# Kernel tuning notes

Hardware: AMD Instinct MI355X
Metric: run time of the kernel (lower is better)

## Reference

```python
import jax, jax.numpy as jnp
import numpy as np

B, QL, DL, RSZ, T = 16, 32, 12, 500, 2
DW, DH = 256, 512
HP = DH // 2  # per-direction GRU hidden
NW, NE = 50000, 100000


def _gru_dir(xp, mask, Wh, bh, reverse):
    # xp: [B, L, 3H'] precomputed input projections; mask: [B, L, 1]
    Hp = Wh.shape[1]
    xp_t = jnp.swapaxes(xp, 0, 1)
    m_t = jnp.swapaxes(mask, 0, 1)
    h0 = jnp.zeros((xp.shape[0], Hp), xp.dtype)

    def step(h, inp):
        x, m = inp
        gh = h @ Wh.T + bh
        r = jax.nn.sigmoid(x[:, :Hp] + gh[:, :Hp])
        z = jax.nn.sigmoid(x[:, Hp:2 * Hp] + gh[:, Hp:2 * Hp])
        n = jnp.tanh(x[:, 2 * Hp:] + r * gh[:, 2 * Hp:])
        hn = (1.0 - z) * n + z * h
        h = m * hn + (1.0 - m) * h  # skip updates at pad tokens
        return h, h

    hT, hs = jax.lax.scan(step, h0, (xp_t, m_t), reverse=reverse)
    return jnp.swapaxes(hs, 0, 1), hT


def _bigru(tokens, emb, Wx, Wh, bx, bh):
    # tokens: [B, L] int, 0 = pad. Wx: [2, 3H', D], Wh: [2, 3H', H'], bx/bh: [2, 3H']
    x = emb[tokens]
    mask = (tokens != 0).astype(x.dtype)[..., None]
    xp_f = jnp.einsum('bld,gd->blg', x, Wx[0]) + bx[0]
    xp_b = jnp.einsum('bld,gd->blg', x, Wx[1]) + bx[1]
    hs_f, hT_f = _gru_dir(xp_f, mask, Wh[0], bh[0], False)
    hs_b, hT_b = _gru_dir(xp_b, mask, Wh[1], bh[1], True)
    word_h = jnp.concatenate([hs_f, hs_b], -1) * mask  # zero pad positions
    sent = jnp.concatenate([hT_f, hT_b], -1)  # last fwd / last bwd hidden
    return word_h, sent


def setup_inputs() -> dict:
    key = jax.random.key(0)
    ks = jax.random.split(key, 12)

    def gru_p(k, din):
        k1, k2 = jax.random.split(k, 2)
        s = 1.0 / float(np.sqrt(HP))
        return (jax.random.normal(k1, (2, 3 * HP, din), jnp.float32) * s,
                jax.random.normal(k2, (2, 3 * HP, HP), jnp.float32) * s,
                jnp.zeros((2, 3 * HP), jnp.float32),
                jnp.zeros((2, 3 * HP), jnp.float32))

    q_Wx, q_Wh, q_bx, q_bh = gru_p(ks[0], DW)
    d_Wx, d_Wh, d_bx, d_bh = gru_p(ks[1], DW)
    kaim = float(np.sqrt(2.0 / DH))
    return {
        'questions': jax.random.randint(ks[2], (B, QL), 0, NW),
        'e_s': jax.random.uniform(ks[3], (B, NE), jnp.float32),
        'pair': jax.random.randint(ks[4], (T, B, RSZ, 2), 0, NE),
        'desc': jax.random.randint(ks[5], (T, B, RSZ, DL), 0, NW),
        'word_emb': jax.random.normal(ks[6], (NW, DW), jnp.float32) * 0.02,
        'q_Wx': q_Wx, 'q_Wh': q_Wh, 'q_bx': q_bx, 'q_bh': q_bh,
        'd_Wx': d_Wx, 'd_Wh': d_Wh, 'd_bx': d_bx, 'd_bh': d_bh,
        'step_W': jax.random.normal(ks[7], (T, DH, DH), jnp.float32) * kaim,
        'step_b': jnp.zeros((T, DH), jnp.float32),
        'rel_W': jax.random.normal(ks[8], (1, DH), jnp.float32) * kaim,
        'rel_b': jnp.zeros((1,), jnp.float32),
        'qcls_W': jax.random.normal(ks[9], (NE, DH), jnp.float32) * kaim,
        'qcls_b': jnp.zeros((NE,), jnp.float32),
    }


def reference(questions, e_s, pair, desc, word_emb, q_Wx, q_Wh, q_bx, q_bh,
              d_Wx, d_Wh, d_bx, d_bh, step_W, step_b, rel_W, rel_b, qcls_W, qcls_b):
    q_word_h, q_emb = _bigru(questions, word_emb, q_Wx, q_Wh, q_bx, q_bh)
    bsz, num_ent = e_s.shape
    last_e = e_s
    for t in range(pair.shape[0]):  # num_steps hops (small, fixed)
        cq = jnp.tanh(q_emb @ step_W[t].T + step_b[t])              # [B,H]
        q_dist = jax.nn.softmax(jnp.einsum('bh,blh->bl', cq, q_word_h), axis=1)
        ctx = jnp.einsum('bl,blh->bh', q_dist, q_word_h)            # [B,H]
        d_tok = desc[t].reshape(-1, desc.shape[-1])                 # [B*rsz, L]
        _, d_emb = _bigru(d_tok, word_emb, d_Wx, d_Wh, d_bx, d_bh)
        d_emb = d_emb.reshape(bsz, -1, d_emb.shape[-1])             # [B,rsz,H]
        d_logit = jnp.einsum('bh,brh,h->br', ctx, d_emb, rel_W[0]) + rel_b[0]
        d_prob = jax.nn.sigmoid(d_logit)                            # [B,rsz]
        sub, obj = pair[t, :, :, 0], pair[t, :, :, 1]
        obj_p = jnp.take_along_axis(last_e, sub, axis=1) * d_prob   # follow: gather
        last_e = jax.vmap(lambda o, p: jnp.zeros((num_ent,), e_s.dtype).at[o].add(p))(obj, obj_p)
        z = jax.lax.stop_gradient(jnp.where(last_e > 1.0, last_e, 1.0))
        last_e = last_e / z
    q_mask = jax.nn.sigmoid(q_emb @ qcls_W.T + qcls_b)
    return last_e * q_mask
```

## Files before the change

### kernel.cpp

```cpp
#include <hip/hip_runtime.h>
#include <math.h>

#define B_    16
#define QL_   32
#define DL_   12
#define RSZ_  500
#define T_    2
#define DW_   256
#define DH_   512
#define HP_   256
#define NW_   50000
#define NE_   100000
#define NSEQD (T_*B_*RSZ_)

typedef _Float16 half8 __attribute__((ext_vector_type(8)));
typedef float   floatx4 __attribute__((ext_vector_type(4)));

__device__ __forceinline__ float sigf(float x){ return 1.0f/(1.0f+expf(-x)); }

__global__ void k_prep_desc(const float* __restrict__ Wx, const float* __restrict__ Wh,
                            _Float16* __restrict__ Bd) {
  int i = blockIdx.x*256 + threadIdx.x;
  int dir = i / 393216;
  int rem = i % 393216;
  float v;
  if (rem < 262144) {
    int n = rem >> 9, k = rem & 511;
    v = (k < 256) ? Wx[(dir*768 + n)*256 + k] : Wh[(dir*768 + n)*256 + (k-256)];
  } else if (rem < 327680) {
    int r2 = rem - 262144; int j = r2 >> 8, k = r2 & 255;
    v = Wx[(dir*768 + 512 + j)*256 + k];
  } else {
    int r2 = rem - 327680; int j = r2 >> 8, k = r2 & 255;
    v = Wh[(dir*768 + 512 + j)*256 + k];
  }
  Bd[i] = (_Float16)v;
}

__global__ void k_prep_qwh(const float* __restrict__ Wh, _Float16* __restrict__ WhQ) {
  int i = blockIdx.x*256 + threadIdx.x;
  WhQ[i] = (_Float16)Wh[i];
}

__global__ __launch_bounds__(256) void k_xproj(
    const int* __restrict__ questions, const float* __restrict__ emb,
    const float* __restrict__ Wx, const float* __restrict__ bx,
    float* __restrict__ xp)
{
  int b = blockIdx.x, n0 = blockIdx.y*128, dir = blockIdx.z;
  int tid = threadIdx.x;
  __shared__ float As[32*256];
  {
    int l = tid >> 3, c8 = tid & 7;
    int tk = questions[b*QL_ + l];
    const float4* src = (const float4*)(emb + (size_t)tk*256) + c8*8;
    float4* dst = (float4*)(As + l*256 + c8*32);
    #pragma unroll
    for (int q = 0; q < 8; ++q) dst[q] = src[q];
  }
  __syncthreads();
  int rr = tid >> 7, jj = tid & 127;
  int n = n0 + jj;
  const float4* W4 = (const float4*)(Wx + ((size_t)dir*768 + n)*256);
  const float4* A4 = (const float4*)As;
  float acc[16];
  #pragma unroll
  for (int i = 0; i < 16; ++i) acc[i] = 0.f;
  for (int k4 = 0; k4 < 64; ++k4) {
    float4 wv = W4[k4];
    #pragma unroll
    for (int i = 0; i < 16; ++i) {
      float4 av = A4[(rr*16 + i)*64 + k4];
      acc[i] += av.x*wv.x + av.y*wv.y + av.z*wv.z + av.w*wv.w;
    }
  }
  float bias = bx[dir*768 + n];
  for (int i = 0; i < 16; ++i)
    xp[(((size_t)dir*16 + b)*QL_ + rr*16 + i)*768 + n] = acc[i] + bias;
}

__global__ __launch_bounds__(512, 2) void k_qgru(
    const int* __restrict__ questions, const _Float16* __restrict__ WhQ,
    const float* __restrict__ bh, const float* __restrict__ xp,
    float* __restrict__ qwh, float* __restrict__ qemb)
{
  const int dir = blockIdx.x;
  const int tid = threadIdx.x;
  const int lane = tid & 63, w = tid >> 6;
  const int lm = lane & 15, lq = lane >> 4;
  const int j0 = w * 32;

  __shared__ _Float16 hA[16*256];
  __shared__ int tokS[16*QL_];

  tokS[tid] = questions[tid];
  {
    int row = tid >> 5, c = tid & 31;
    half8 z8 = {0,0,0,0,0,0,0,0};
    *(half8*)(hA + row*256 + (c ^ row)*8) = z8;
  }

  half8 Bq[3][2][8];
  #pragma unroll
  for (int g = 0; g < 3; ++g)
    #pragma unroll
    for (int f = 0; f < 2; ++f)
      #pragma unroll
      for (int kf = 0; kf < 8; ++kf) {
        int row = g*256 + j0 + f*16 + lm;
        Bq[g][f][kf] = *(const half8*)(WhQ + ((size_t)dir*768 + row)*256 + kf*32 + lq*8);
      }
  float bh_r[2], bh_z[2], bh_n[2];
  #pragma unroll
  for (int f = 0; f < 2; ++f) {
    int j = j0 + f*16 + lm;
    bh_r[f] = bh[dir*768 + j];
    bh_z[f] = bh[dir*768 + 256 + j];
    bh_n[f] = bh[dir*768 + 512 + j];
  }
  float hreg[2][4];
  #pragma unroll
  for (int f = 0; f < 2; ++f)
    #pragma unroll
    for (int r = 0; r < 4; ++r) hreg[f][r] = 0.f;

  __syncthreads();

  for (int t = 0; t < QL_; ++t) {
    int l = dir ? (QL_-1-t) : t;
    floatx4 aR[2], aZ[2], aG[2];
    #pragma unroll
    for (int f = 0; f < 2; ++f) {
      floatx4 z4 = {0.f,0.f,0.f,0.f};
      aR[f]=z4; aZ[f]=z4; aG[f]=z4;
    }
    #pragma unroll
    for (int kf = 0; kf < 8; ++kf) {
      int p = (kf*4 + lq) ^ lm;
      half8 a = *(const half8*)(hA + lm*256 + p*8);
      #pragma unroll
      for (int f = 0; f < 2; ++f) {
        aR[f] = __builtin_amdgcn_mfma_f32_16x16x32_f16(a, Bq[0][f][kf], aR[f], 0,0,0);
        aZ[f] = __builtin_amdgcn_mfma_f32_16x16x32_f16(a, Bq[1][f][kf], aZ[f], 0,0,0);
        aG[f] = __builtin_amdgcn_mfma_f32_16x16x32_f16(a, Bq[2][f][kf], aG[f], 0,0,0);
      }
    }
    __syncthreads();

    #pragma unroll
    for (int f = 0; f < 2; ++f) {
      int j = j0 + f*16 + lm;
      #pragma unroll
      for (int reg = 0; reg < 4; ++reg) {
        int b = lq*4 + reg;
        const float* xpb = xp + (((size_t)dir*16 + b)*QL_ + l)*768;
        float r  = sigf(xpb[j]       + aR[f][reg] + bh_r[f]);
        float z  = sigf(xpb[256 + j] + aZ[f][reg] + bh_z[f]);
        float nt = tanhf(xpb[512 + j] + r*(aG[f][reg] + bh_n[f]));
        float hold = hreg[f][reg];
        float hn = (1.f - z)*nt + z*hold;
        int tk = tokS[b*QL_ + l];
        float hnew = (tk != 0) ? hn : hold;
        hreg[f][reg] = hnew;
        int p2 = ((j >> 3) ^ b);
        hA[b*256 + p2*8 + (j & 7)] = (_Float16)hnew;
        qwh[((size_t)b*QL_ + l)*512 + dir*256 + j] = (tk != 0) ? hnew : 0.f;
      }
    }
    __syncthreads();
  }
  #pragma unroll
  for (int f = 0; f < 2; ++f) {
    int j = j0 + f*16 + lm;
    #pragma unroll
    for (int reg = 0; reg < 4; ++reg) {
      int b = lq*4 + reg;
      qemb[b*512 + dir*256 + j] = hreg[f][reg];
    }
  }
}

__global__ __launch_bounds__(1024, 4) void k_desc_gru(
    const int* __restrict__ desc, const float* __restrict__ emb,
    const _Float16* __restrict__ Bd, const float* __restrict__ bx,
    const float* __restrict__ bh, float* __restrict__ dh)
{
  const int dir  = blockIdx.z;
  const int seq0 = blockIdx.x * 64;
  const int tid  = threadIdx.x;
  const int lane = tid & 63, w = tid >> 6;
  const int lm = lane & 15, lq = lane >> 4;
  const int j0 = w * 16;
  const int rot = blockIdx.x & 7;

  __shared__ _Float16 A2[64*512];

  {
    int row = tid >> 4, cc = tid & 15;
    half8 z8 = {0,0,0,0,0,0,0,0};
    #pragma unroll
    for (int q = 0; q < 2; ++q) {
      int c = 32 + cc*2 + q;
      *(half8*)(A2 + row*512 + (c ^ row)*8) = z8;
    }
  }

  const int l0 = dir ? (DL_-1) : 0;
  const int dl = dir ? -1 : 1;

  auto stage_x = [&](int ll) {
    int row = tid >> 4, cc = tid & 15;
    int s = seq0 + row;
    int tk = desc[(size_t)s*DL_ + ll];
    const float4* src = (const float4*)(emb + (size_t)tk*256);
    #pragma unroll
    for (int q = 0; q < 2; ++q) {
      int c = cc*2 + q;
      float4 v0 = src[c*2], v1 = src[c*2+1];
      half8 hv;
      hv[0]=(_Float16)v0.x; hv[1]=(_Float16)v0.y; hv[2]=(_Float16)v0.z; hv[3]=(_Float16)v0.w;
      hv[4]=(_Float16)v1.x; hv[5]=(_Float16)v1.y; hv[6]=(_Float16)v1.z; hv[7]=(_Float16)v1.w;
      *(half8*)(A2 + row*512 + (c ^ row)*8) = hv;
    }
  };
  stage_x(l0);

  const _Float16* Bdir = Bd + (size_t)dir * 393216;
  const _Float16* Brz  = Bdir;
  const _Float16* Bxn  = Bdir + 262144;
  const _Float16* Bgn  = Bdir + 327680;

  const int jl = j0 + lm;
  const float bias_r = bx[dir*768 + jl]       + bh[dir*768 + jl];
  const float bias_z = bx[dir*768 + 256 + jl] + bh[dir*768 + 256 + jl];
  const float bias_n = bx[dir*768 + 512 + jl];
  const float bias_g = bh[dir*768 + 512 + jl];

  int l = l0;
  for (int t = 0; t < DL_; ++t, l += dl) {
    __syncthreads();

    floatx4 accR[4], accZ[4], accN[4], accG[4];
    #pragma unroll
    for (int mi = 0; mi < 4; ++mi) {
      floatx4 z4 = {0.f,0.f,0.f,0.f};
      accR[mi]=z4; accZ[mi]=z4; accN[mi]=z4; accG[mi]=z4;
    }

    #pragma unroll
    for (int half = 0; half < 2; ++half) {
      #pragma unroll 2
      for (int kk = 0; kk < 8; ++kk) {
        int kfx = half*8 + ((kk + rot) & 7);
        int k0 = kfx*32 + lq*8;
        half8 br = *(const half8*)(Brz + (size_t)jl*512 + k0);
        half8 bz = *(const half8*)(Brz + (size_t)(256 + jl)*512 + k0);
        half8 bb = half ? *(const half8*)(Bgn + (size_t)jl*256 + (k0 - 256))
                        : *(const half8*)(Bxn + (size_t)jl*256 + k0);
        int cb = kfx*4 + lq;
        #pragma unroll
        for (int mi = 0; mi < 4; ++mi) {
          int row = mi*16 + lm;
          half8 a = *(const half8*)(A2 + row*512 + (cb ^ row)*8);
          accR[mi] = __builtin_amdgcn_mfma_f32_16x16x32_f16(a, br, accR[mi], 0,0,0);
          accZ[mi] = __builtin_amdgcn_mfma_f32_16x16x32_f16(a, bz, accZ[mi], 0,0,0);
          if (half) accG[mi] = __builtin_amdgcn_mfma_f32_16x16x32_f16(a, bb, accG[mi], 0,0,0);
          else      accN[mi] = __builtin_amdgcn_mfma_f32_16x16x32_f16(a, bb, accN[mi], 0,0,0);
        }
      }
    }

    __syncthreads();

    #pragma unroll
    for (int mi = 0; mi < 4; ++mi) {
      #pragma unroll
      for (int reg = 0; reg < 4; ++reg) {
        int m = mi*16 + lq*4 + reg;
        float r  = sigf(accR[mi][reg] + bias_r);
        float z  = sigf(accZ[mi][reg] + bias_z);
        float nt = tanhf(accN[mi][reg] + bias_n + r*(accG[mi][reg] + bias_g));
        int c2 = 32 + (jl >> 3);
        _Float16* hp = A2 + m*512 + ((c2 ^ m)*8) + (jl & 7);
        float hold = (float)(*hp);
        float hn = (1.f - z)*nt + z*hold;
        int tk = desc[(size_t)(seq0 + m)*DL_ + l];
        float hnew = (tk != 0) ? hn : hold;
        *hp = (_Float16)hnew;
        if (t == DL_-1)
          dh[((size_t)dir*NSEQD + seq0 + m)*256 + jl] = hnew;
      }
    }
    if (t < DL_-1) stage_x(l + dl);
  }
}

__global__ __launch_bounds__(256) void k_attn(
    const float* __restrict__ qemb, const float* __restrict__ qwh,
    const float* __restrict__ sW, const float* __restrict__ sb,
    const float* __restrict__ relW, float* __restrict__ u, int t)
{
  int b = blockIdx.x, tid = threadIdx.x;
  __shared__ float qe[512];
  __shared__ float cq[512];
  __shared__ float lg[32];
  __shared__ float dist[32];
  qe[tid]     = qemb[b*512 + tid];
  qe[tid+256] = qemb[b*512 + 256 + tid];
  __syncthreads();
  const float4* qe4 = (const float4*)qe;
  for (int nn = 0; nn < 2; ++nn) {
    int n = tid + nn*256;
    const float4* w4 = (const float4*)(sW + ((size_t)t*512 + n)*512);
    float acc = 0.f;
    for (int k4 = 0; k4 < 128; ++k4) {
      float4 w = w4[k4]; float4 q = qe4[k4];
      acc += w.x*q.x + w.y*q.y + w.z*q.z + w.w*q.w;
    }
    cq[n] = tanhf(acc + sb[t*512 + n]);
  }
  __syncthreads();
  if (tid < 32) {
    const float4* r4 = (const float4*)(qwh + ((size_t)b*QL_ + tid)*512);
    const float4* c4 = (const float4*)cq;
    float acc = 0.f;
    for (int k4 = 0; k4 < 128; ++k4) {
      float4 w = r4[k4]; float4 q = c4[k4];
      acc += w.x*q.x + w.y*q.y + w.z*q.z + w.w*q.w;
    }
    lg[tid] = acc;
  }
  __syncthreads();
  if (tid == 0) {
    float mx = lg[0];
    for (int i = 1; i < 32; ++i) mx = fmaxf(mx, lg[i]);
    float s = 0.f;
    for (int i = 0; i < 32; ++i) { float e = expf(lg[i]-mx); dist[i] = e; s += e; }
    float inv = 1.f/s;
    for (int i = 0; i < 32; ++i) dist[i] *= inv;
  }
  __syncthreads();
  for (int nn = 0; nn < 2; ++nn) {
    int c = tid + nn*256;
    float acc = 0.f;
    #pragma unroll 4
    for (int ll = 0; ll < 32; ++ll)
      acc += dist[ll] * qwh[((size_t)b*QL_ + ll)*512 + c];
    u[b*512 + c] = acc * relW[c];
  }
}

__global__ __launch_bounds__(256) void k_dlogit(
    const float* __restrict__ u, const float* __restrict__ dh,
    const float* __restrict__ relb, float* __restrict__ dprob, int t)
{
  int w = threadIdx.x >> 6, lane = threadIdx.x & 63;
  int o = blockIdx.x*4 + w;
  int b = o / 500;
  int s = t*(B_*RSZ_) + o;
  const float* e0 = dh + (size_t)s*256;
  const float* e1 = dh + (size_t)NSEQD*256 + (size_t)s*256;
  float acc = 0.f;
  #pragma unroll
  for (int i = 0; i < 4; ++i) {
    int c = lane + i*64;
    acc += u[b*512 + c]       * e0[c];
    acc += u[b*512 + 256 + c] * e1[c];
  }
  #pragma unroll
  for (int off = 32; off; off >>= 1) acc += __shfl_down(acc, off);
  if (lane == 0) dprob[o] = sigf(acc + relb[0]);
}

__global__ void k_scatter(const int* __restrict__ pair, const float* __restrict__ dprob,
                          const float* __restrict__ esrc, float* __restrict__ edst,
                          int t, int clampflag)
{
  int o = blockIdx.x*256 + threadIdx.x;
  if (o >= B_*RSZ_) return;
  int b = o / RSZ_, r = o % RSZ_;
  const int* pp = pair + (((size_t)t*B_ + b)*RSZ_ + r)*2;
  int sub = pp[0], obj = pp[1];
  float v = esrc[(size_t)b*NE_ + sub];
  if (clampflag) v = fminf(v, 1.0f);
  atomicAdd(edst + (size_t)b*NE_ + obj, v * dprob[o]);
}

__global__ __launch_bounds__(256) void k_final(
    const float* __restrict__ qemb, const float* __restrict__ W,
    const float* __restrict__ bias, const float* __restrict__ efin,
    float* __restrict__ out)
{
  int tid = threadIdx.x;
  int lane = tid & 63;
  int ks = lane & 15, bg = lane >> 4;
  int b = (tid >> 6)*4 + bg;
  float q[32];
  {
    const float4* q4 = (const float4*)(qemb + b*512 + ks*32);
    #pragma unroll
    for (int i = 0; i < 8; ++i) {
      float4 v = q4[i];
      q[4*i]=v.x; q[4*i+1]=v.y; q[4*i+2]=v.z; q[4*i+3]=v.w;
    }
  }
  int e0 = blockIdx.x*256;
  int eend = (e0+256 < NE_) ? e0+256 : NE_;
  for (int e = e0; e < eend; ++e) {
    const float4* w4 = (const float4*)(W + (size_t)e*512 + ks*32);
    float acc = 0.f;
    #pragma unroll
    for (int i = 0; i < 8; ++i) {
      float4 v = w4[i];
      acc += v.x*q[4*i] + v.y*q[4*i+1] + v.z*q[4*i+2] + v.w*q[4*i+3];
    }
    acc += __shfl_xor(acc, 1);
    acc += __shfl_xor(acc, 2);
    acc += __shfl_xor(acc, 4);
    acc += __shfl_xor(acc, 8);
    if (ks == 0) {
      float msk = sigf(acc + bias[e]);
      float ev = fminf(efin[(size_t)b*NE_ + e], 1.0f);
      out[(size_t)b*NE_ + e] = ev * msk;
    }
  }
}

extern "C" void kernel_launch(void* const* d_in, const int* in_sizes, int n_in,
                              void* d_out, int out_size, void* d_ws, size_t ws_size,
                              hipStream_t stream)
{
  const int*   questions = (const int*)d_in[0];
  const float* e_s   = (const float*)d_in[1];
  const int*   pair  = (const int*)d_in[2];
  const int*   desc  = (const int*)d_in[3];
  const float* emb   = (const float*)d_in[4];
  const float* qWx   = (const float*)d_in[5];
  const float* qWh   = (const float*)d_in[6];
  const float* qbx   = (const float*)d_in[7];
  const float* qbh   = (const float*)d_in[8];
  const float* dWx   = (const float*)d_in[9];
  const float* dWh   = (const float*)d_in[10];
  const float* dbx   = (const float*)d_in[11];
  const float* dbh   = (const float*)d_in[12];
  const float* stepW = (const float*)d_in[13];
  const float* stepb = (const float*)d_in[14];
  const float* relW  = (const float*)d_in[15];
  const float* relb  = (const float*)d_in[16];
  const float* qclsW = (const float*)d_in[17];
  const float* qclsb = (const float*)d_in[18];
  float* out = (float*)d_out;

  char* ws = (char*)d_ws;
  size_t off = 0;
  auto alloc = [&](size_t bytes)->void* {
    void* p = ws + off; off += (bytes + 255) & ~(size_t)255; return p;
  };
  _Float16* Bd   = (_Float16*)alloc((size_t)2*393216*sizeof(_Float16));
  _Float16* WhQ  = (_Float16*)alloc((size_t)2*768*256*sizeof(_Float16));
  float* xp   = (float*)alloc((size_t)2*16*QL_*768*sizeof(float));
  float* qemb = (float*)alloc((size_t)16*512*sizeof(float));
  float* qwh  = (float*)alloc((size_t)16*QL_*512*sizeof(float));
  float* dh   = (float*)alloc((size_t)2*NSEQD*256*sizeof(float));
  float* u    = (float*)alloc((size_t)16*512*sizeof(float));
  float* dprob= (float*)alloc((size_t)B_*RSZ_*sizeof(float));
  float* ebuf = (float*)alloc((size_t)2*B_*NE_*sizeof(float));

  hipMemsetAsync(ebuf, 0, (size_t)2*B_*NE_*sizeof(float), stream);

  k_prep_desc<<<3072, 256, 0, stream>>>(dWx, dWh, Bd);
  k_prep_qwh<<<1536, 256, 0, stream>>>(qWh, WhQ);

  k_xproj<<<dim3(16,6,2), 256, 0, stream>>>(questions, emb, qWx, qbx, xp);
  k_qgru<<<2, 512, 0, stream>>>(questions, WhQ, qbh, xp, qwh, qemb);

  k_desc_gru<<<dim3(250,1,2), 1024, 0, stream>>>(desc, emb, Bd, dbx, dbh, dh);

  for (int t = 0; t < T_; ++t) {
    k_attn<<<16, 256, 0, stream>>>(qemb, qwh, stepW, stepb, relW, u, t);
    k_dlogit<<<2000, 256, 0, stream>>>(u, dh, relb, dprob, t);
    const float* esrc = (t == 0) ? e_s : ebuf;
    float* edst = ebuf + (size_t)t*B_*NE_;
    k_scatter<<<32, 256, 0, stream>>>(pair, dprob, esrc, edst, t, t);
  }
  k_final<<<(NE_+255)/256, 256, 0, stream>>>(qemb, qclsW, qclsb, ebuf + (size_t)B_*NE_, out);
}
```

Baseline: 2.059 ms.

## Use fast sigmoid/tanh intrinsics and restructure question GRU with 1024 threads

Replaces expf/tanhf with __expf plus hardware reciprocal approximations in all GRU and attention kernels. The question GRU moves to 1024 threads, reloads weight fragments from global each step instead of keeping them in registers, and stages per-step x-projections into shared memory after a layout change to [dir][l][b]. The description GRU caches tokens in shared memory, drops its per-block k-rotation and unrolls its inner loop more. These cut transcendental cost and global reads on the serial recurrence, but the approximations are less accurate and the question GRU now issues more global weight loads every step.

```diff
diff --git a/kernel.cpp b/kernel.cpp
--- a/kernel.cpp
+++ b/kernel.cpp
@@ -16,7 +16,12 @@
 typedef _Float16 half8 __attribute__((ext_vector_type(8)));
 typedef float   floatx4 __attribute__((ext_vector_type(4)));
 
-__device__ __forceinline__ float sigf(float x){ return 1.0f/(1.0f+expf(-x)); }
+__device__ __forceinline__ float sigf(float x){
+  return __builtin_amdgcn_rcpf(1.0f + __expf(-x));
+}
+__device__ __forceinline__ float tanhfast(float x){
+  return 1.0f - 2.0f*__builtin_amdgcn_rcpf(1.0f + __expf(2.0f*x));
+}
 
 __global__ void k_prep_desc(const float* __restrict__ Wx, const float* __restrict__ Wh,
                             _Float16* __restrict__ Bd) {
@@ -75,11 +80,13 @@
     }
   }
   float bias = bx[dir*768 + n];
-  for (int i = 0; i < 16; ++i)
-    xp[(((size_t)dir*16 + b)*QL_ + rr*16 + i)*768 + n] = acc[i] + bias;
-}
-
-__global__ __launch_bounds__(512, 2) void k_qgru(
+  for (int i = 0; i < 16; ++i) {
+    int l = rr*16 + i;
+    xp[(((size_t)dir*QL_ + l)*16 + b)*768 + n] = acc[i] + bias;
+  }
+}
+
+__global__ __launch_bounds__(1024, 4) void k_qgru(
     const int* __restrict__ questions, const _Float16* __restrict__ WhQ,
     const float* __restrict__ bh, const float* __restrict__ xp,
     float* __restrict__ qwh, float* __restrict__ qemb)
@@ -88,95 +95,75 @@
   const int tid = threadIdx.x;
   const int lane = tid & 63, w = tid >> 6;
   const int lm = lane & 15, lq = lane >> 4;
-  const int j0 = w * 32;
+  const int jl = w*16 + lm;
 
   __shared__ _Float16 hA[16*256];
-  __shared__ int tokS[16*QL_];
-
-  tokS[tid] = questions[tid];
-  {
+  __shared__ float xpL[2][16*768];
+  __shared__ int tokS[512];
+
+  if (tid < 512) {
+    tokS[tid] = questions[tid];
     int row = tid >> 5, c = tid & 31;
     half8 z8 = {0,0,0,0,0,0,0,0};
     *(half8*)(hA + row*256 + (c ^ row)*8) = z8;
   }
 
-  half8 Bq[3][2][8];
-  #pragma unroll
-  for (int g = 0; g < 3; ++g)
-    #pragma unroll
-    for (int f = 0; f < 2; ++f)
-      #pragma unroll
-      for (int kf = 0; kf < 8; ++kf) {
-        int row = g*256 + j0 + f*16 + lm;
-        Bq[g][f][kf] = *(const half8*)(WhQ + ((size_t)dir*768 + row)*256 + kf*32 + lq*8);
-      }
-  float bh_r[2], bh_z[2], bh_n[2];
-  #pragma unroll
-  for (int f = 0; f < 2; ++f) {
-    int j = j0 + f*16 + lm;
-    bh_r[f] = bh[dir*768 + j];
-    bh_z[f] = bh[dir*768 + 256 + j];
-    bh_n[f] = bh[dir*768 + 512 + j];
-  }
-  float hreg[2][4];
-  #pragma unroll
-  for (int f = 0; f < 2; ++f)
-    #pragma unroll
-    for (int r = 0; r < 4; ++r) hreg[f][r] = 0.f;
-
-  __syncthreads();
+  const _Float16* pR = WhQ + ((size_t)dir*768 + jl)*256;
+  const _Float16* pZ = WhQ + ((size_t)dir*768 + 256 + jl)*256;
+  const _Float16* pG = WhQ + ((size_t)dir*768 + 512 + jl)*256;
+  const float bh_r = bh[dir*768 + jl];
+  const float bh_z = bh[dir*768 + 256 + jl];
+  const float bh_n = bh[dir*768 + 512 + jl];
+  float hreg[4] = {0.f,0.f,0.f,0.f};
 
   for (int t = 0; t < QL_; ++t) {
     int l = dir ? (QL_-1-t) : t;
-    floatx4 aR[2], aZ[2], aG[2];
-    #pragma unroll
-    for (int f = 0; f < 2; ++f) {
-      floatx4 z4 = {0.f,0.f,0.f,0.f};
-      aR[f]=z4; aZ[f]=z4; aG[f]=z4;
-    }
+    int par = t & 1;
+    {
+      const float4* src = (const float4*)(xp + (((size_t)dir*QL_ + l)*16)*768);
+      float4* dst = (float4*)xpL[par];
+      dst[tid]        = src[tid];
+      dst[tid + 1024] = src[tid + 1024];
+      dst[tid + 2048] = src[tid + 2048];
+    }
+    __syncthreads();
+
+    floatx4 aR = {0,0,0,0}, aZ = {0,0,0,0}, aG = {0,0,0,0};
     #pragma unroll
     for (int kf = 0; kf < 8; ++kf) {
       int p = (kf*4 + lq) ^ lm;
       half8 a = *(const half8*)(hA + lm*256 + p*8);
-      #pragma unroll
-      for (int f = 0; f < 2; ++f) {
-        aR[f] = __builtin_amdgcn_mfma_f32_16x16x32_f16(a, Bq[0][f][kf], aR[f], 0,0,0);
-        aZ[f] = __builtin_amdgcn_mfma_f32_16x16x32_f16(a, Bq[1][f][kf], aZ[f], 0,0,0);
-        aG[f] = __builtin_amdgcn_mfma_f32_16x16x32_f16(a, Bq[2][f][kf], aG[f], 0,0,0);
-      }
+      int k0 = kf*32 + lq*8;
+      half8 br = *(const half8*)(pR + k0);
+      half8 bz = *(const half8*)(pZ + k0);
+      half8 bg = *(const half8*)(pG + k0);
+      aR = __builtin_amdgcn_mfma_f32_16x16x32_f16(a, br, aR, 0,0,0);
+      aZ = __builtin_amdgcn_mfma_f32_16x16x32_f16(a, bz, aZ, 0,0,0);
+      aG = __builtin_amdgcn_mfma_f32_16x16x32_f16(a, bg, aG, 0,0,0);
     }
     __syncthreads();
 
-    #pragma unroll
-    for (int f = 0; f < 2; ++f) {
-      int j = j0 + f*16 + lm;
-      #pragma unroll
-      for (int reg = 0; reg < 4; ++reg) {
-        int b = lq*4 + reg;
-        const float* xpb = xp + (((size_t)dir*16 + b)*QL_ + l)*768;
-        float r  = sigf(xpb[j]       + aR[f][reg] + bh_r[f]);
-        float z  = sigf(xpb[256 + j] + aZ[f][reg] + bh_z[f]);
-        float nt = tanhf(xpb[512 + j] + r*(aG[f][reg] + bh_n[f]));
-        float hold = hreg[f][reg];
-        float hn = (1.f - z)*nt + z*hold;
-        int tk = tokS[b*QL_ + l];
-        float hnew = (tk != 0) ? hn : hold;
-        hreg[f][reg] = hnew;
-        int p2 = ((j >> 3) ^ b);
-        hA[b*256 + p2*8 + (j & 7)] = (_Float16)hnew;
-        qwh[((size_t)b*QL_ + l)*512 + dir*256 + j] = (tk != 0) ? hnew : 0.f;
-      }
-    }
-    __syncthreads();
-  }
-  #pragma unroll
-  for (int f = 0; f < 2; ++f) {
-    int j = j0 + f*16 + lm;
     #pragma unroll
     for (int reg = 0; reg < 4; ++reg) {
       int b = lq*4 + reg;
-      qemb[b*512 + dir*256 + j] = hreg[f][reg];
-    }
+      const float* xb = &xpL[par][b*768];
+      float r  = sigf(xb[jl]       + aR[reg] + bh_r);
+      float z  = sigf(xb[256 + jl] + aZ[reg] + bh_z);
+      float nt = tanhfast(xb[512 + jl] + r*(aG[reg] + bh_n));
+      float hold = hreg[reg];
+      float hn = (1.f - z)*nt + z*hold;
+      int tk = tokS[b*QL_ + l];
+      float hnew = (tk != 0) ? hn : hold;
+      hreg[reg] = hnew;
+      int p2 = (jl >> 3) ^ b;
+      hA[b*256 + p2*8 + (jl & 7)] = (_Float16)hnew;
+      qwh[((size_t)b*QL_ + l)*512 + dir*256 + jl] = (tk != 0) ? hnew : 0.f;
+    }
+  }
+  #pragma unroll
+  for (int reg = 0; reg < 4; ++reg) {
+    int b = lq*4 + reg;
+    qemb[b*512 + dir*256 + jl] = hreg[reg];
   }
 }
 
@@ -191,9 +178,9 @@
   const int lane = tid & 63, w = tid >> 6;
   const int lm = lane & 15, lq = lane >> 4;
   const int j0 = w * 16;
-  const int rot = blockIdx.x & 7;
 
   __shared__ _Float16 A2[64*512];
+  __shared__ int tokL[2][64];
 
   {
     int row = tid >> 4, cc = tid & 15;
@@ -208,10 +195,11 @@
   const int l0 = dir ? (DL_-1) : 0;
   const int dl = dir ? -1 : 1;
 
-  auto stage_x = [&](int ll) {
+  auto stage_x = [&](int ll, int par) {
     int row = tid >> 4, cc = tid & 15;
     int s = seq0 + row;
     int tk = desc[(size_t)s*DL_ + ll];
+    if (cc == 0) tokL[par][row] = tk;
     const float4* src = (const float4*)(emb + (size_t)tk*256);
     #pragma unroll
     for (int q = 0; q < 2; ++q) {
@@ -223,14 +211,15 @@
       *(half8*)(A2 + row*512 + (c ^ row)*8) = hv;
     }
   };
-  stage_x(l0);
+  stage_x(l0, 0);
 
   const _Float16* Bdir = Bd + (size_t)dir * 393216;
-  const _Float16* Brz  = Bdir;
-  const _Float16* Bxn  = Bdir + 262144;
-  const _Float16* Bgn  = Bdir + 327680;
-
   const int jl = j0 + lm;
+  const _Float16* pR = Bdir + (size_t)jl*512;
+  const _Float16* pZ = Bdir + (size_t)(256 + jl)*512;
+  const _Float16* pX = Bdir + 262144 + (size_t)jl*256;
+  const _Float16* pG = Bdir + 327680 + (size_t)jl*256;
+
   const float bias_r = bx[dir*768 + jl]       + bh[dir*768 + jl];
   const float bias_z = bx[dir*768 + 256 + jl] + bh[dir*768 + 256 + jl];
   const float bias_n = bx[dir*768 + 512 + jl];
@@ -249,14 +238,14 @@
 
     #pragma unroll
     for (int half = 0; half < 2; ++half) {
-      #pragma unroll 2
+      #pragma unroll 4
       for (int kk = 0; kk < 8; ++kk) {
-        int kfx = half*8 + ((kk + rot) & 7);
+        int kfx = half*8 + kk;
         int k0 = kfx*32 + lq*8;
-        half8 br = *(const half8*)(Brz + (size_t)jl*512 + k0);
-        half8 bz = *(const half8*)(Brz + (size_t)(256 + jl)*512 + k0);
-        half8 bb = half ? *(const half8*)(Bgn + (size_t)jl*256 + (k0 - 256))
-                        : *(const half8*)(Bxn + (size_t)jl*256 + k0);
+        half8 br = *(const half8*)(pR + k0);
+        half8 bz = *(const half8*)(pZ + k0);
+        half8 bb = half ? *(const half8*)(pG + (k0 - 256))
+                        : *(const half8*)(pX + k0);
         int cb = kfx*4 + lq;
         #pragma unroll
         for (int mi = 0; mi < 4; ++mi) {
@@ -272,6 +261,7 @@
 
     __syncthreads();
 
+    int par = t & 1;
     #pragma unroll
     for (int mi = 0; mi < 4; ++mi) {
       #pragma unroll
@@ -279,19 +269,19 @@
         int m = mi*16 + lq*4 + reg;
         float r  = sigf(accR[mi][reg] + bias_r);
         float z  = sigf(accZ[mi][reg] + bias_z);
-        float nt = tanhf(accN[mi][reg] + bias_n + r*(accG[mi][reg] + bias_g));
+        float nt = tanhfast(accN[mi][reg] + bias_n + r*(accG[mi][reg] + bias_g));
         int c2 = 32 + (jl >> 3);
         _Float16* hp = A2 + m*512 + ((c2 ^ m)*8) + (jl & 7);
         float hold = (float)(*hp);
         float hn = (1.f - z)*nt + z*hold;
-        int tk = desc[(size_t)(seq0 + m)*DL_ + l];
+        int tk = tokL[par][m];
         float hnew = (tk != 0) ? hn : hold;
         *hp = (_Float16)hnew;
         if (t == DL_-1)
           dh[((size_t)dir*NSEQD + seq0 + m)*256 + jl] = hnew;
       }
     }
-    if (t < DL_-1) stage_x(l + dl);
+    if (t < DL_-1) stage_x(l + dl, (t+1) & 1);
   }
 }
 
@@ -317,7 +307,7 @@
       float4 w = w4[k4]; float4 q = qe4[k4];
       acc += w.x*q.x + w.y*q.y + w.z*q.z + w.w*q.w;
     }
-    cq[n] = tanhf(acc + sb[t*512 + n]);
+    cq[n] = tanhfast(acc + sb[t*512 + n]);
   }
   __syncthreads();
   if (tid < 32) {
@@ -335,8 +325,8 @@
     float mx = lg[0];
     for (int i = 1; i < 32; ++i) mx = fmaxf(mx, lg[i]);
     float s = 0.f;
-    for (int i = 0; i < 32; ++i) { float e = expf(lg[i]-mx); dist[i] = e; s += e; }
-    float inv = 1.f/s;
+    for (int i = 0; i < 32; ++i) { float e = __expf(lg[i]-mx); dist[i] = e; s += e; }
+    float inv = __builtin_amdgcn_rcpf(s);
     for (int i = 0; i < 32; ++i) dist[i] *= inv;
   }
   __syncthreads();
@@ -458,7 +448,7 @@
   };
   _Float16* Bd   = (_Float16*)alloc((size_t)2*393216*sizeof(_Float16));
   _Float16* WhQ  = (_Float16*)alloc((size_t)2*768*256*sizeof(_Float16));
-  float* xp   = (float*)alloc((size_t)2*16*QL_*768*sizeof(float));
+  float* xp   = (float*)alloc((size_t)2*QL_*16*768*sizeof(float));
   float* qemb = (float*)alloc((size_t)16*512*sizeof(float));
   float* qwh  = (float*)alloc((size_t)16*QL_*512*sizeof(float));
   float* dh   = (float*)alloc((size_t)2*NSEQD*256*sizeof(float));
@@ -472,7 +462,7 @@
   k_prep_qwh<<<1536, 256, 0, stream>>>(qWh, WhQ);
 
   k_xproj<<<dim3(16,6,2), 256, 0, stream>>>(questions, emb, qWx, qbx, xp);
-  k_qgru<<<2, 512, 0, stream>>>(questions, WhQ, qbh, xp, qwh, qemb);
+  k_qgru<<<2, 1024, 0, stream>>>(questions, WhQ, qbh, xp, qwh, qemb);
 
   k_desc_gru<<<dim3(250,1,2), 1024, 0, stream>>>(desc, emb, Bd, dbx, dbh, dh);
 
```

After: 1.834 ms. 1.12x faster.
